# Kernel tuning notes

Measured on AMD Instinct MI355X. Metric: run time of the kernel, lower is better.

## Reference

```python
import jax, jax.numpy as jnp
import numpy as np


def setup_inputs() -> dict:
    key = jax.random.key(0)
    k0, k1, k2, k3, k4 = jax.random.split(key, 5)
    K, LENGTH, D, B, MAXDEPTH = 50000, 65536, 128, 1024, 16
    weights = jax.random.normal(k0, (LENGTH, D), dtype=jnp.float32)
    x = jax.random.normal(k1, (B, D), dtype=jnp.float32)
    y = jax.random.randint(k2, (B,), 0, K, dtype=jnp.int64)
    # padded per-class paths of internal (pseudo-class) nodes; real paths index [K, LENGTH)
    path_idx = jax.random.randint(k3, (K, MAXDEPTH), 0, LENGTH, dtype=jnp.int64)
    path_len = jax.random.randint(k4, (K,), 0, MAXDEPTH, dtype=jnp.int32)
    return {"weights": weights, "x": x, "y": y, "path_idx": path_idx, "path_len": path_len}


def reference(weights, x, y, path_idx, path_len):
    # weights: [LENGTH, d]; x: [B, d]; y: [B]; path_idx: [K, Dmax]; path_len: [K]
    K, Dmax = path_idx.shape
    # mask out padded path slots (original loops over len(path)-1 real ancestors)
    mask = (jnp.arange(Dmax)[None, :] < path_len[:, None]).astype(weights.dtype)  # [K, Dmax]
    # gather ancestor rows and sum along the path; add the class's own row j
    path_sum = jnp.einsum("kpd,kp->kd", weights[path_idx], mask)  # [K, d]
    added_weights = weights[:K] + path_sum                        # [K, d]
    logits = x @ added_weights.T                                  # [B, K]
    logp = jax.nn.log_softmax(logits, axis=-1)
    loss = -jnp.take_along_axis(logp, y[:, None], axis=1).mean()  # CrossEntropyLoss (mean)
    return loss, logits, added_weights
```

## Files before the change

kernel.cpp:

```cpp
#include <hip/hip_runtime.h>
#include <math.h>

#define KCLS  50000
#define KP    50048
#define DIM   128
#define BATCH 1024
#define MAXD  16

typedef __attribute__((ext_vector_type(8))) short short8;
typedef __attribute__((ext_vector_type(4))) float floatx4;

__device__ __forceinline__ unsigned short f2bf(float f) {
    unsigned u = __float_as_uint(f);
    u += 0x7fffu + ((u >> 16) & 1u);
    return (unsigned short)(u >> 16);
}

__global__ __launch_bounds__(256) void aw_kernel(
    const float* __restrict__ weights, const int* __restrict__ path_idx,
    const int* __restrict__ path_len, float* __restrict__ aw,
    unsigned short* __restrict__ awb)
{
    int t = threadIdx.x;
    int c = t >> 5;
    int lane = t & 31;
    int k = blockIdx.x * 8 + c;
    int col = lane * 4;

    if (k >= KCLS) {
        ushort4 z = {0, 0, 0, 0};
        *(ushort4*)(awb + (size_t)k * DIM + col) = z;
        return;
    }

    float4 acc = *(const float4*)(weights + (size_t)k * DIM + col);
    int len = path_len[k];
    const int* pp = path_idx + (size_t)k * MAXD;
    for (int p = 0; p < len; ++p) {
        int idx = pp[p];
        float4 wv = *(const float4*)(weights + (size_t)idx * DIM + col);
        acc.x += wv.x; acc.y += wv.y; acc.z += wv.z; acc.w += wv.w;
    }
    *(float4*)(aw + (size_t)k * DIM + col) = acc;
    ushort4 hv = { f2bf(acc.x), f2bf(acc.y), f2bf(acc.z), f2bf(acc.w) };
    *(ushort4*)(awb + (size_t)k * DIM + col) = hv;
}

__global__ __launch_bounds__(256) void xconv_kernel(
    const float* __restrict__ x, unsigned short* __restrict__ xb)
{
    int i = (blockIdx.x * 256 + threadIdx.x) * 4;
    float4 v = *(const float4*)(x + i);
    ushort4 hv = { f2bf(v.x), f2bf(v.y), f2bf(v.z), f2bf(v.w) };
    *(ushort4*)(xb + i) = hv;
}

__global__ __launch_bounds__(256) void gemm_kernel(
    const unsigned short* __restrict__ Xb,
    const unsigned short* __restrict__ Wb,
    float* __restrict__ logits)
{
    int tid = threadIdx.x;
    int wave = tid >> 6, lane = tid & 63;
    int r = lane & 15, quad = lane >> 4;
    int m0 = blockIdx.y * 128 + (wave >> 1) * 64;
    int n0 = blockIdx.x * 128 + (wave & 1) * 64;

    const unsigned short* ap = Xb + (size_t)(m0 + r) * DIM + quad * 8;
    const unsigned short* bp = Wb + (size_t)(n0 + r) * DIM + quad * 8;

    floatx4 acc[4][4];
    #pragma unroll
    for (int i = 0; i < 4; ++i)
        #pragma unroll
        for (int j = 0; j < 4; ++j)
            acc[i][j] = (floatx4){0.f, 0.f, 0.f, 0.f};

    #pragma unroll
    for (int kk = 0; kk < 4; ++kk) {
        short8 a[4], b[4];
        #pragma unroll
        for (int i = 0; i < 4; ++i)
            a[i] = *(const short8*)(ap + (size_t)(i * 16) * DIM + kk * 32);
        #pragma unroll
        for (int j = 0; j < 4; ++j)
            b[j] = *(const short8*)(bp + (size_t)(j * 16) * DIM + kk * 32);
        #pragma unroll
        for (int i = 0; i < 4; ++i)
            #pragma unroll
            for (int j = 0; j < 4; ++j)
                acc[i][j] = __builtin_amdgcn_mfma_f32_16x16x32_bf16(
                    a[i], b[j], acc[i][j], 0, 0, 0);
    }

    #pragma unroll
    for (int i = 0; i < 4; ++i) {
        int mrow = m0 + i * 16 + quad * 4;
        #pragma unroll
        for (int j = 0; j < 4; ++j) {
            int col = n0 + j * 16 + r;
            if (col < KCLS) {
                float* cp = logits + (size_t)mrow * KCLS + col;
                #pragma unroll
                for (int reg = 0; reg < 4; ++reg)
                    cp[(size_t)reg * KCLS] = acc[i][j][reg];
            }
        }
    }
}

__global__ __launch_bounds__(256) void lse_kernel(
    const float* __restrict__ logits, const int* __restrict__ y,
    float* __restrict__ loss)
{
    int b = blockIdx.x;
    const float* row = logits + (size_t)b * KCLS;
    float m = -INFINITY, s = 0.f;

    auto upd = [&](float v) {
        if (v <= m) {
            s += __expf(v - m);
        } else {
            s = s * __expf(m - v) + 1.f;
            m = v;
        }
    };

    if (threadIdx.x < 3) upd(row[threadIdx.x]);
    const float4* rv = (const float4*)(row + 3);
    for (int i = threadIdx.x; i < 12499; i += 256) {
        float4 v = rv[i];
        upd(v.x); upd(v.y); upd(v.z); upd(v.w);
    }
    if (threadIdx.x == 3) upd(row[49999]);

    #pragma unroll
    for (int off = 32; off > 0; off >>= 1) {
        float m2 = __shfl_down(m, off);
        float s2 = __shfl_down(s, off);
        float M = fmaxf(m, m2);
        s = s * __expf(m - M) + s2 * __expf(m2 - M);
        m = M;
    }
    __shared__ float sm[4], ss[4];
    int w = threadIdx.x >> 6, l = threadIdx.x & 63;
    if (l == 0) { sm[w] = m; ss[w] = s; }
    __syncthreads();
    if (threadIdx.x == 0) {
        m = sm[0]; s = ss[0];
        #pragma unroll
        for (int i = 1; i < 4; ++i) {
            float M = fmaxf(m, sm[i]);
            s = s * __expf(m - M) + ss[i] * __expf(sm[i] - M);
            m = M;
        }
        float lse = m + __logf(s);
        float ly = row[y[b]];
        atomicAdd(loss, (lse - ly) * (1.0f / BATCH));
    }
}

extern "C" void kernel_launch(void* const* d_in, const int* in_sizes, int n_in,
                              void* d_out, int out_size, void* d_ws, size_t ws_size,
                              hipStream_t stream)
{
    const float* weights  = (const float*)d_in[0];
    const float* x        = (const float*)d_in[1];
    const int*   y        = (const int*)d_in[2];
    const int*   path_idx = (const int*)d_in[3];
    const int*   path_len = (const int*)d_in[4];

    float* out    = (float*)d_out;
    float* loss   = out;
    float* logits = out + 1;
    float* aw     = out + 1 + (size_t)BATCH * KCLS;

    unsigned short* awb = (unsigned short*)d_ws;
    unsigned short* xb  = awb + (size_t)KP * DIM;

    hipMemsetAsync(loss, 0, sizeof(float), stream);

    aw_kernel<<<KP / 8, 256, 0, stream>>>(weights, path_idx, path_len, aw, awb);
    xconv_kernel<<<BATCH * DIM / 1024, 256, 0, stream>>>(x, xb);

    gemm_kernel<<<dim3(KP / 128, BATCH / 128), 256, 0, stream>>>(xb, awb, logits);

    lse_kernel<<<BATCH, 256, 0, stream>>>(logits, y, loss);
}
```

Before: 385.1 us.

## Fuse per-tile softmax partials into GEMM epilogue and merge x conversion into aw kernel

The GEMM epilogue now computes a per-row (max, sum-exp) partial for each 64-column wave tile and writes it to a workspace buffer. A small reduction kernel then combines those partials, so the full logits matrix no longer has to be re-read for log-sum-exp. The x-to-bf16 conversion is folded into the aw kernel as extra blocks, and aw uses one wave per class with float2 lanes and a two-way unrolled path loop. The fused path needs extra workspace and falls back to the old kernels when the workspace is too small.

```diff
diff --git a/kernel.cpp b/kernel.cpp
--- a/kernel.cpp
+++ b/kernel.cpp
@@ -7,6 +7,11 @@
 #define BATCH 1024
 #define MAXD  16
 
+#define NBLK_N   (KP / 128)
+#define NBP      (NBLK_N * 2)
+#define CLS_BLOCKS (KP / 4)
+#define XB_BLOCKS  (BATCH * DIM / 1024)
+
 typedef __attribute__((ext_vector_type(8))) short short8;
 typedef __attribute__((ext_vector_type(4))) float floatx4;
 
@@ -19,46 +24,59 @@
 __global__ __launch_bounds__(256) void aw_kernel(
     const float* __restrict__ weights, const int* __restrict__ path_idx,
     const int* __restrict__ path_len, float* __restrict__ aw,
-    unsigned short* __restrict__ awb)
+    unsigned short* __restrict__ awb,
+    const float* __restrict__ x, unsigned short* __restrict__ xb)
 {
     int t = threadIdx.x;
-    int c = t >> 5;
-    int lane = t & 31;
-    int k = blockIdx.x * 8 + c;
-    int col = lane * 4;
+
+    if (blockIdx.x >= CLS_BLOCKS) {
+        int i = ((blockIdx.x - CLS_BLOCKS) * 256 + t) * 4;
+        float4 v = *(const float4*)(x + i);
+        ushort4 hv = { f2bf(v.x), f2bf(v.y), f2bf(v.z), f2bf(v.w) };
+        *(ushort4*)(xb + i) = hv;
+        return;
+    }
+
+    int w = t >> 6, lane = t & 63;
+    int k = blockIdx.x * 4 + w;
+    int col = lane * 2;
 
     if (k >= KCLS) {
-        ushort4 z = {0, 0, 0, 0};
-        *(ushort4*)(awb + (size_t)k * DIM + col) = z;
+        ushort2 z; z.x = 0; z.y = 0;
+        *(ushort2*)(awb + (size_t)k * DIM + col) = z;
         return;
     }
 
-    float4 acc = *(const float4*)(weights + (size_t)k * DIM + col);
+    float2 acc = *(const float2*)(weights + (size_t)k * DIM + col);
     int len = path_len[k];
     const int* pp = path_idx + (size_t)k * MAXD;
-    for (int p = 0; p < len; ++p) {
-        int idx = pp[p];
-        float4 wv = *(const float4*)(weights + (size_t)idx * DIM + col);
-        acc.x += wv.x; acc.y += wv.y; acc.z += wv.z; acc.w += wv.w;
-    }
-    *(float4*)(aw + (size_t)k * DIM + col) = acc;
-    ushort4 hv = { f2bf(acc.x), f2bf(acc.y), f2bf(acc.z), f2bf(acc.w) };
-    *(ushort4*)(awb + (size_t)k * DIM + col) = hv;
-}
-
-__global__ __launch_bounds__(256) void xconv_kernel(
-    const float* __restrict__ x, unsigned short* __restrict__ xb)
-{
-    int i = (blockIdx.x * 256 + threadIdx.x) * 4;
-    float4 v = *(const float4*)(x + i);
-    ushort4 hv = { f2bf(v.x), f2bf(v.y), f2bf(v.z), f2bf(v.w) };
-    *(ushort4*)(xb + i) = hv;
-}
-
+
+    int p = 0;
+    for (; p + 2 <= len; p += 2) {
+        int i0 = pp[p], i1 = pp[p + 1];
+        float2 a = *(const float2*)(weights + (size_t)i0 * DIM + col);
+        float2 b = *(const float2*)(weights + (size_t)i1 * DIM + col);
+        acc.x += a.x + b.x;
+        acc.y += a.y + b.y;
+    }
+    if (p < len) {
+        int i0 = pp[p];
+        float2 a = *(const float2*)(weights + (size_t)i0 * DIM + col);
+        acc.x += a.x;
+        acc.y += a.y;
+    }
+
+    *(float2*)(aw + (size_t)k * DIM + col) = acc;
+    ushort2 hv; hv.x = f2bf(acc.x); hv.y = f2bf(acc.y);
+    *(ushort2*)(awb + (size_t)k * DIM + col) = hv;
+}
+
+template<bool PART>
 __global__ __launch_bounds__(256) void gemm_kernel(
     const unsigned short* __restrict__ Xb,
     const unsigned short* __restrict__ Wb,
-    float* __restrict__ logits)
+    float* __restrict__ logits,
+    float2* __restrict__ part)
 {
     int tid = threadIdx.x;
     int wave = tid >> 6, lane = tid & 63;
@@ -96,6 +114,7 @@
     #pragma unroll
     for (int i = 0; i < 4; ++i) {
         int mrow = m0 + i * 16 + quad * 4;
+
         #pragma unroll
         for (int j = 0; j < 4; ++j) {
             int col = n0 + j * 16 + r;
@@ -106,6 +125,63 @@
                     cp[(size_t)reg * KCLS] = acc[i][j][reg];
             }
         }
+
+        if constexpr (PART) {
+            #pragma unroll
+            for (int reg = 0; reg < 4; ++reg) {
+                float v[4];
+                #pragma unroll
+                for (int j = 0; j < 4; ++j) {
+                    int col = n0 + j * 16 + r;
+                    v[j] = (col < KCLS) ? acc[i][j][reg] : -INFINITY;
+                }
+                float mx = fmaxf(fmaxf(v[0], v[1]), fmaxf(v[2], v[3]));
+                #pragma unroll
+                for (int off = 8; off; off >>= 1)
+                    mx = fmaxf(mx, __shfl_xor(mx, off));
+                float s = __expf(v[0] - mx) + __expf(v[1] - mx)
+                        + __expf(v[2] - mx) + __expf(v[3] - mx);
+                #pragma unroll
+                for (int off = 8; off; off >>= 1)
+                    s += __shfl_xor(s, off);
+                if (r == 0)
+                    part[(size_t)(mrow + reg) * NBP + blockIdx.x * 2 + (wave & 1)]
+                        = make_float2(mx, s);
+            }
+        }
+    }
+}
+
+__global__ __launch_bounds__(256) void lsereduce_kernel(
+    const float2* __restrict__ part, const float* __restrict__ logits,
+    const int* __restrict__ y, float* __restrict__ loss)
+{
+    int b = blockIdx.x * 4 + (threadIdx.x >> 6);
+    int lane = threadIdx.x & 63;
+    const float2* pr = part + (size_t)b * NBP;
+
+    float m = -INFINITY, s = 0.f;
+    for (int i = lane; i < NBP; i += 64) {
+        float2 pv = pr[i];
+        if (pv.x > m) {
+            s = s * __expf(m - pv.x) + pv.y;
+            m = pv.x;
+        } else {
+            s += pv.y * __expf(pv.x - m);
+        }
+    }
+    #pragma unroll
+    for (int off = 32; off; off >>= 1) {
+        float m2 = __shfl_xor(m, off);
+        float s2 = __shfl_xor(s, off);
+        float M = fmaxf(m, m2);
+        s = s * __expf(m - M) + s2 * __expf(m2 - M);
+        m = M;
+    }
+    if (lane == 0) {
+        float lse = m + __logf(s);
+        float ly = logits[(size_t)b * KCLS + y[b]];
+        atomicAdd(loss, (lse - ly) * (1.0f / BATCH));
     }
 }
 
@@ -175,15 +251,27 @@
     float* logits = out + 1;
     float* aw     = out + 1 + (size_t)BATCH * KCLS;
 
+    size_t awb_sz  = (size_t)KP * DIM * sizeof(unsigned short);
+    size_t xb_sz   = (size_t)BATCH * DIM * sizeof(unsigned short);
+    size_t part_sz = (size_t)BATCH * NBP * sizeof(float2);
+
     unsigned short* awb = (unsigned short*)d_ws;
     unsigned short* xb  = awb + (size_t)KP * DIM;
+    float2* part = (float2*)((char*)d_ws + awb_sz + xb_sz);
+    bool fused = ws_size >= awb_sz + xb_sz + part_sz;
 
     hipMemsetAsync(loss, 0, sizeof(float), stream);
 
-    aw_kernel<<<KP / 8, 256, 0, stream>>>(weights, path_idx, path_len, aw, awb);
-    xconv_kernel<<<BATCH * DIM / 1024, 256, 0, stream>>>(x, xb);
-
-    gemm_kernel<<<dim3(KP / 128, BATCH / 128), 256, 0, stream>>>(xb, awb, logits);
-
-    lse_kernel<<<BATCH, 256, 0, stream>>>(logits, y, loss);
-}
+    aw_kernel<<<CLS_BLOCKS + XB_BLOCKS, 256, 0, stream>>>(
+        weights, path_idx, path_len, aw, awb, x, xb);
+
+    if (fused) {
+        gemm_kernel<true><<<dim3(NBLK_N, BATCH / 128), 256, 0, stream>>>(
+            xb, awb, logits, part);
+        lsereduce_kernel<<<BATCH / 4, 256, 0, stream>>>(part, logits, y, loss);
+    } else {
+        gemm_kernel<false><<<dim3(NBLK_N, BATCH / 128), 256, 0, stream>>>(
+            xb, awb, logits, nullptr);
+        lse_kernel<<<BATCH, 256, 0, stream>>>(logits, y, loss);
+    }
+}
```

Result: slower. 400.3 us (+4.0%).
